# Performance work log

Measured on AMD Instinct MI355X. Metric: run time of the kernel, lower is better.

## Reference

```python
import jax, jax.numpy as jnp
import numpy as np
import math

B, S, HID = 2, 2048, 2048
NH, NKV, HD = 16, 4, 128
N_REP = NH // NKV
THETA = 1000000.0


def apply_rope(x, position_ids, theta=THETA):
    # x: (B, H, S, D), position_ids: (B, S)
    d = x.shape[-1]
    freqs = 1.0 / (theta ** (jnp.arange(0, d, 2, dtype=jnp.float32) / d))  # (D/2,)
    angles = position_ids.astype(jnp.float32)[:, :, None] * freqs[None, None, :]  # (B,S,D/2)
    cos = jnp.cos(angles)[:, None, :, :]  # (B,1,S,D/2)
    sin = jnp.sin(angles)[:, None, :, :]
    x_even = x[..., 0::2]
    x_odd = x[..., 1::2]
    rot_even = x_even * cos - x_odd * sin
    rot_odd = x_even * sin + x_odd * cos
    out = jnp.stack([rot_even, rot_odd], axis=-1)  # (B,H,S,D/2,2)
    return out.reshape(x.shape)


def setup_inputs() -> dict:
    key = jax.random.key(0)
    ks = jax.random.split(key, 6)
    x = jax.random.normal(ks[0], (B, S, HID), dtype=jnp.float32)
    position_ids = jnp.broadcast_to(jnp.arange(S, dtype=jnp.int64)[None, :], (B, S))
    # causal additive mask: 0 on/below diagonal, large negative above
    causal = jnp.where(jnp.tril(jnp.ones((S, S), dtype=bool)), 0.0, -1e9).astype(jnp.float32)
    attention_mask = jnp.broadcast_to(causal[None, None, :, :], (B, 1, S, S))
    sc = 1.0 / math.sqrt(HID)
    Wq = jax.random.normal(ks[1], (HID, NH * HD), dtype=jnp.float32) * sc
    Wk = jax.random.normal(ks[2], (HID, NKV * HD), dtype=jnp.float32) * sc
    Wv = jax.random.normal(ks[3], (HID, NKV * HD), dtype=jnp.float32) * sc
    Wo = jax.random.normal(ks[4], (NH * HD, HID), dtype=jnp.float32) * sc
    return {"x": x, "position_ids": position_ids, "attention_mask": attention_mask,
            "Wq": Wq, "Wk": Wk, "Wv": Wv, "Wo": Wo}


def reference(x, position_ids, attention_mask, Wq, Wk, Wv, Wo):
    b, s, _ = x.shape
    q = (x @ Wq).reshape(b, s, NH, HD).transpose(0, 2, 1, 3)   # (B,NH,S,D)
    k = (x @ Wk).reshape(b, s, NKV, HD).transpose(0, 2, 1, 3)  # (B,NKV,S,D)
    v = (x @ Wv).reshape(b, s, NKV, HD).transpose(0, 2, 1, 3)
    q = apply_rope(q, position_ids)
    k = apply_rope(k, position_ids)
    # repeat_kv: expand KV heads to match Q heads
    k = jnp.repeat(k, N_REP, axis=1)  # (B,NH,S,D)
    v = jnp.repeat(v, N_REP, axis=1)
    scale = 1.0 / math.sqrt(HD)
    scores = jnp.einsum('bhqd,bhkd->bhqk', q, k) * scale
    scores = scores + attention_mask
    attn = jax.nn.softmax(scores, axis=-1)
    out = jnp.einsum('bhqk,bhkd->bhqd', attn, v)
    out = out.transpose(0, 2, 1, 3).reshape(b, s, NH * HD)
    return out @ Wo
```

## Files before the change

### kernel.cpp

```cpp
#include <hip/hip_runtime.h>
#include <hip/hip_bf16.h>

#define S_LEN 2048
#define HID_D 2048
#define NH 16
#define NKV 4
#define HD 128
#define BATCH 2

typedef __hip_bfloat16 bf16;
using f32x4 = __attribute__((ext_vector_type(4))) float;
using s16x8 = __attribute__((ext_vector_type(8))) short;

struct TrueT { static constexpr bool value = true; };
struct FalseT { static constexpr bool value = false; };

__device__ __forceinline__ f32x4 mfma_16x16x32(s16x8 a, s16x8 b, f32x4 c) {
  return __builtin_amdgcn_mfma_f32_16x16x32_bf16(a, b, c, 0, 0, 0);
}

__device__ __forceinline__ void gload16(const void* g, void* l) {
  __builtin_amdgcn_global_load_lds(
      (const __attribute__((address_space(1))) void*)g,
      (__attribute__((address_space(3))) void*)l, 16, 0, 0);
}

__device__ __forceinline__ unsigned int pk2bf(float a, float b) {
  __hip_bfloat16 lo = __float2bfloat16(a), hi = __float2bfloat16(b);
  return ((unsigned int)*(unsigned short*)&hi << 16) | *(unsigned short*)&lo;
}

__global__ __launch_bounds__(256) void prep_k(const float* __restrict__ x,
                                              const float* __restrict__ Wq,
                                              const float* __restrict__ Wk,
                                              const float* __restrict__ Wv,
                                              const float* __restrict__ Wo,
                                              bf16* __restrict__ xb,
                                              bf16* __restrict__ WqkvT,
                                              bf16* __restrict__ WoT) {
  __shared__ float tile[32][33];
  const int tid = threadIdx.x;
  const int X = blockIdx.x;
  if (X < 10240) {
    const int bx = X % 160, by = X / 160;
    const float* src;
    bf16* dst;
    int N, n0;
    if (bx < 64) { src = Wq; dst = WqkvT; N = 2048; n0 = bx * 32; }
    else if (bx < 80) { src = Wk; dst = WqkvT + (size_t)2048 * 2048; N = 512; n0 = (bx - 64) * 32; }
    else if (bx < 96) { src = Wv; dst = WqkvT + (size_t)2560 * 2048; N = 512; n0 = (bx - 80) * 32; }
    else { src = Wo; dst = WoT; N = 2048; n0 = (bx - 96) * 32; }
    const int k0 = by * 32;
    const int tx = tid & 31, ty = tid >> 5;
#pragma unroll
    for (int i = ty; i < 32; i += 8) tile[i][tx] = src[(size_t)(k0 + i) * N + n0 + tx];
    __syncthreads();
#pragma unroll
    for (int i = ty; i < 32; i += 8)
      dst[(size_t)(n0 + i) * 2048 + k0 + tx] = __float2bfloat16(tile[tx][i]);
  } else {
    int i = ((X - 10240) * 256 + tid) * 4;
    float4 v = *(const float4*)&x[i];
    xb[i + 0] = __float2bfloat16(v.x);
    xb[i + 1] = __float2bfloat16(v.y);
    xb[i + 2] = __float2bfloat16(v.z);
    xb[i + 3] = __float2bfloat16(v.w);
  }
}

__global__ __launch_bounds__(512) void gemm256_k(const bf16* __restrict__ A,
                                                 const bf16* __restrict__ Bt,
                                                 bf16* __restrict__ C,
                                                 int M, int N, int K) {
  __shared__ bf16 Asm[2][256 * 64];
  __shared__ bf16 Bsm[2][256 * 64];
  const int tid = threadIdx.x;
  const int lane = tid & 63, wid = tid >> 6;
  const int fr = lane & 15, hi = lane >> 4;

  const int bid = blockIdx.y * gridDim.x + blockIdx.x;
  const int nwg = gridDim.x * gridDim.y;
  const int swz = (bid & 7) * (nwg >> 3) + (bid >> 3);
  const int m0 = (swz % gridDim.x) * 256;
  const int n0 = (swz / gridDim.x) * 256;

  const bf16* Ag = A + (size_t)m0 * K;
  const bf16* Bg = Bt + (size_t)n0 * K;

  auto stageT = [&](const bf16* src, bf16* ldsBase, int k0) {
#pragma unroll
    for (int c = 0; c < 4; ++c) {
      int byte = tid * 16 + c * 8192;
      int row = byte >> 7;
      int col = byte & 127;
      int colSw = col ^ ((row & 7) << 4);
      gload16((const char*)(src + (size_t)row * K + k0) + colSw,
              (char*)ldsBase + byte);
    }
  };

  f32x4 acc[4][8];
#pragma unroll
  for (int m = 0; m < 4; ++m)
#pragma unroll
    for (int n = 0; n < 8; ++n) acc[m][n] = (f32x4){0.f, 0.f, 0.f, 0.f};

  const int r0 = (wid >> 1) * 64;
  const int c0 = (wid & 1) * 128;
  const int NT = K >> 6;

  stageT(Ag, &Asm[0][0], 0);
  stageT(Bg, &Bsm[0][0], 0);
  asm volatile("s_waitcnt vmcnt(0)" ::: "memory");
  __builtin_amdgcn_s_barrier();

  for (int t = 0; t < NT; ++t) {
    const int cur = t & 1;
    const int nxt = cur ^ 1;
    const int kn = (t + 1) << 6;
    const bool more = (t + 1) < NT;
#pragma unroll
    for (int p = 0; p < 2; ++p) {
      s16x8 af[4], bq[8];
#pragma unroll
      for (int m = 0; m < 4; ++m) {
        int r = r0 + m * 16 + fr;
        int cb = (p * 64 + hi * 16) ^ ((r & 7) << 4);
        af[m] = *(const s16x8*)((const char*)&Asm[cur][0] + r * 128 + cb);
      }
#pragma unroll
      for (int n = 0; n < 8; ++n) {
        int bn = c0 + n * 16 + fr;
        int cb = (p * 64 + hi * 16) ^ ((bn & 7) << 4);
        bq[n] = *(const s16x8*)((const char*)&Bsm[cur][0] + bn * 128 + cb);
      }
      if (p == 0) {
        if (more) {
          stageT(Ag, &Asm[nxt][0], kn);
          stageT(Bg, &Bsm[nxt][0], kn);
        }
      } else {
        asm volatile("s_waitcnt vmcnt(0)" ::: "memory");
      }
      __builtin_amdgcn_s_barrier();

      __builtin_amdgcn_s_setprio(1);
#pragma unroll
      for (int m = 0; m < 4; ++m)
#pragma unroll
        for (int n = 0; n < 8; ++n)
          acc[m][n] = mfma_16x16x32(af[m], bq[n], acc[m][n]);
      __builtin_amdgcn_s_setprio(0);
    }
  }

#pragma unroll
  for (int m = 0; m < 4; ++m)
#pragma unroll
    for (int n = 0; n < 8; ++n) {
      const int row = m0 + r0 + m * 16 + hi * 4;
      const int col = n0 + c0 + n * 16 + fr;
#pragma unroll
      for (int r = 0; r < 4; ++r)
        C[(size_t)(row + r) * N + col] = __float2bfloat16(acc[m][n][r]);
    }
}

__global__ __launch_bounds__(256) void gemm128sq_k(const bf16* __restrict__ A,
                                                   const bf16* __restrict__ Bt,
                                                   float* __restrict__ C,
                                                   int M, int N, int K) {
  __shared__ bf16 Asm[2][128 * 64];
  __shared__ bf16 Bsm[2][128 * 64];
  const int tid = threadIdx.x;
  const int lane = tid & 63, wid = tid >> 6;
  const int fr = lane & 15, hi = lane >> 4;

  const int bid = blockIdx.y * gridDim.x + blockIdx.x;
  const int nwg = gridDim.x * gridDim.y;
  const int swz = (bid & 7) * (nwg >> 3) + (bid >> 3);
  const int m0 = (swz % gridDim.x) * 128;
  const int n0 = (swz / gridDim.x) * 128;

  const bf16* Ag = A + (size_t)m0 * K;
  const bf16* Bg = Bt + (size_t)n0 * K;

  auto stageT = [&](const bf16* src, bf16* ldsBase, int k0) {
#pragma unroll
    for (int c = 0; c < 4; ++c) {
      int byte = tid * 16 + c * 4096;
      int row = byte >> 7;
      int col = byte & 127;
      int colSw = col ^ ((row & 7) << 4);
      gload16((const char*)(src + (size_t)row * K + k0) + colSw,
              (char*)ldsBase + byte);
    }
  };

  f32x4 acc[4][4];
#pragma unroll
  for (int m = 0; m < 4; ++m)
#pragma unroll
    for (int n = 0; n < 4; ++n) acc[m][n] = (f32x4){0.f, 0.f, 0.f, 0.f};

  const int r0 = (wid >> 1) * 64;
  const int c0 = (wid & 1) * 64;
  const int NT = K >> 6;

  stageT(Ag, &Asm[0][0], 0);
  stageT(Bg, &Bsm[0][0], 0);
  asm volatile("s_waitcnt vmcnt(0)" ::: "memory");
  __builtin_amdgcn_s_barrier();

  for (int t = 0; t < NT; ++t) {
    const int cur = t & 1;
    const int nxt = cur ^ 1;
    const int kn = (t + 1) << 6;
    const bool more = (t + 1) < NT;
#pragma unroll
    for (int p = 0; p < 2; ++p) {
      s16x8 af[4], bq[4];
#pragma unroll
      for (int m = 0; m < 4; ++m) {
        int r = r0 + m * 16 + fr;
        int cb = (p * 64 + hi * 16) ^ ((r & 7) << 4);
        af[m] = *(const s16x8*)((const char*)&Asm[cur][0] + r * 128 + cb);
      }
#pragma unroll
      for (int n = 0; n < 4; ++n) {
        int bn = c0 + n * 16 + fr;
        int cb = (p * 64 + hi * 16) ^ ((bn & 7) << 4);
        bq[n] = *(const s16x8*)((const char*)&Bsm[cur][0] + bn * 128 + cb);
      }
      if (p == 0) {
        if (more) {
          stageT(Ag, &Asm[nxt][0], kn);
          stageT(Bg, &Bsm[nxt][0], kn);
        }
      } else {
        asm volatile("s_waitcnt vmcnt(0)" ::: "memory");
      }
      __builtin_amdgcn_s_barrier();

      __builtin_amdgcn_s_setprio(1);
#pragma unroll
      for (int m = 0; m < 4; ++m)
#pragma unroll
        for (int n = 0; n < 4; ++n)
          acc[m][n] = mfma_16x16x32(af[m], bq[n], acc[m][n]);
      __builtin_amdgcn_s_setprio(0);
    }
  }

#pragma unroll
  for (int m = 0; m < 4; ++m)
#pragma unroll
    for (int n = 0; n < 4; ++n) {
      const int row = m0 + r0 + m * 16 + hi * 4;
      const int col = n0 + c0 + n * 16 + fr;
#pragma unroll
      for (int r = 0; r < 4; ++r)
        C[(size_t)(row + r) * N + col] = acc[m][n][r];
    }
}

__global__ __launch_bounds__(256) void postq_k(const bf16* __restrict__ qkv,
                                               const int* __restrict__ pos_ids,
                                               bf16* __restrict__ Q,
                                               bf16* __restrict__ Kd,
                                               bf16* __restrict__ Vt) {
  __shared__ unsigned short vtile[32][33];
  const int tid = threadIdx.x;
  const int X = blockIdx.x;
  const float kscale = 0.12751841418861862f;

  if (X < 16384) {
    int idx = X * 256 + tid;
    int i = idx & 63;
    int h = (idx >> 6) & 15;
    int s = (idx >> 10) & 2047;
    int b = idx >> 21;
    float pos = (float)pos_ids[b * S_LEN + s];
    float freq = exp2f((float)i * -0.31143075889569023f);
    float ang = pos * freq;
    float sn, cs;
    sincosf(ang, &sn, &cs);
    const bf16* src = qkv + (size_t)(b * S_LEN + s) * 3072 + h * HD + 2 * i;
    float e = __bfloat162float(src[0]), o = __bfloat162float(src[1]);
    bf16* dst = Q + ((size_t)(b * NH + h) * S_LEN + s) * HD + 2 * i;
    dst[0] = __float2bfloat16((e * cs - o * sn) * kscale);
    dst[1] = __float2bfloat16((e * sn + o * cs) * kscale);
  } else if (X < 20480) {
    int idx = (X - 16384) * 256 + tid;
    int i = idx & 63;
    int kvh = (idx >> 6) & 3;
    int s = (idx >> 8) & 2047;
    int b = idx >> 19;
    float pos = (float)pos_ids[b * S_LEN + s];
    float freq = exp2f((float)i * -0.31143075889569023f);
    float ang = pos * freq;
    float sn, cs;
    sincosf(ang, &sn, &cs);
    const bf16* src = qkv + (size_t)(b * S_LEN + s) * 3072 + 2048 + kvh * HD + 2 * i;
    float e = __bfloat162float(src[0]), o = __bfloat162float(src[1]);
    bf16* dst = Kd + ((size_t)(b * NKV + kvh) * S_LEN + s) * HD + 2 * i;
    dst[0] = __float2bfloat16(e * cs - o * sn);
    dst[1] = __float2bfloat16(e * sn + o * cs);
  } else {
    const int vb = X - 20480;
    const int s0 = (vb & 63) * 32;
    const int d0 = ((vb >> 6) & 3) * 32;
    const int z = vb >> 8;
    const int b = z >> 2, kvh = z & 3;
    const int tx = tid & 31, ty = tid >> 5;
    const unsigned short* src = (const unsigned short*)qkv + 2560 + kvh * HD;
#pragma unroll
    for (int i = ty; i < 32; i += 8)
      vtile[i][tx] = src[(size_t)(b * S_LEN + s0 + i) * 3072 + d0 + tx];
    __syncthreads();
    unsigned short* dst = (unsigned short*)Vt + (size_t)(b * NKV + kvh) * HD * S_LEN;
#pragma unroll
    for (int i = ty; i < 32; i += 8)
      dst[(size_t)(d0 + i) * S_LEN + s0 + tx] = vtile[tx][i];
  }
}

__global__ __launch_bounds__(256) void attn_k(const bf16* __restrict__ Q,
                                              const bf16* __restrict__ K,
                                              const bf16* __restrict__ Vt,
                                              bf16* __restrict__ Aout) {
  __shared__ bf16 Ks[2][64 * 128];
  __shared__ bf16 Vs[2][128 * 64];
  __shared__ bf16 Ps[4][16 * 64];

  const int lane = threadIdx.x & 63;
  const int wid = threadIdx.x >> 6;
  const int fr = lane & 15;
  const int hi = lane >> 4;
  const int pi = blockIdx.x, h = blockIdx.y, b = blockIdx.z;
  const int kvh = h >> 2;
  const bf16* Qh = Q + (size_t)(b * NH + h) * S_LEN * HD;
  const bf16* Kh = K + (size_t)(b * NKV + kvh) * S_LEN * HD;
  const bf16* Vh = Vt + (size_t)(b * NKV + kvh) * HD * S_LEN;

  const int oB = lane * 16;
  const int rinK = oB >> 8;
  const int rinV = oB >> 7;
  bf16* myP = &Ps[wid][0];
  const int pswz = (fr & 7) << 4;

  auto stageKV = [&](int bufi, int kv0) {
#pragma unroll
    for (int c = 0; c < 4; ++c) {
      int absr = wid * 16 + c * 4 + rinK;
      int colb = (oB & 255) ^ (((absr >> 2) & 7) << 4);
      gload16((const char*)Kh + (size_t)(kv0 + absr) * 256 + colb,
              (char*)&Ks[bufi][0] + (wid * 16 + c * 4) * 256);
    }
#pragma unroll
    for (int c = 0; c < 4; ++c) {
      int absd = wid * 32 + c * 8 + rinV;
      int colb = (oB & 127) ^ ((absd & 7) << 4);
      gload16((const char*)Vh + (size_t)absd * (S_LEN * 2) + (size_t)kv0 * 2 + colb,
              (char*)&Vs[bufi][0] + (wid * 32 + c * 8) * 128);
    }
  };

#pragma unroll 1
  for (int t = 0; t < 2; ++t) {
    const int qb = t ? (31 - pi) : pi;
    const int q0w = qb * 64 + wid * 16;
    const int nsteps = qb + 1;

    s16x8 qf[4];
#pragma unroll
    for (int ks = 0; ks < 4; ++ks)
      qf[ks] = *(const s16x8*)&Qh[(size_t)(q0w + fr) * HD + ks * 32 + hi * 8];

    f32x4 o[8];
#pragma unroll
    for (int ds = 0; ds < 8; ++ds) o[ds] = (f32x4){0.f, 0.f, 0.f, 0.f};
    float lacc[4];
#pragma unroll
    for (int r = 0; r < 4; ++r) lacc[r] = 0.f;

    auto doStep = [&](int kv0, int bufc, auto LASTC) {
      constexpr bool LAST = decltype(LASTC)::value;
      f32x4 sg[4];
#pragma unroll
      for (int kv = 0; kv < 4; ++kv) {
        f32x4 a = (f32x4){0.f, 0.f, 0.f, 0.f};
        const int row = 4 * fr + kv;
#pragma unroll
        for (int ks = 0; ks < 4; ++ks) {
          int cb = (ks * 64 + hi * 16) ^ (((row >> 2) & 7) << 4);
          s16x8 kf = *(const s16x8*)((const char*)&Ks[bufc][0] + row * 256 + cb);
          a = mfma_16x16x32(qf[ks], kf, a);
        }
        sg[kv] = a;
      }

#pragma unroll
      for (int r = 0; r < 4; ++r) {
        float p0 = __builtin_exp2f(sg[0][r]);
        float p1 = __builtin_exp2f(sg[1][r]);
        float p2 = __builtin_exp2f(sg[2][r]);
        float p3 = __builtin_exp2f(sg[3][r]);
        if (LAST) {
          const int qrow = q0w + hi * 4 + r;
          const int kb = kv0 + 4 * fr;
          p0 = (kb <= qrow) ? p0 : 0.f;
          p1 = (kb + 1 <= qrow) ? p1 : 0.f;
          p2 = (kb + 2 <= qrow) ? p2 : 0.f;
          p3 = (kb + 3 <= qrow) ? p3 : 0.f;
        }
        lacc[r] += (p0 + p1) + (p2 + p3);
        const int prow = hi * 4 + r;
        uint2 pv;
        pv.x = pk2bf(p0, p1);
        pv.y = pk2bf(p2, p3);
        *(uint2*)((char*)myP + prow * 128 + ((fr * 8) ^ ((prow & 7) << 4))) = pv;
      }
      __builtin_amdgcn_wave_barrier();

      s16x8 pf[2];
#pragma unroll
      for (int g = 0; g < 2; ++g) {
        int cb = (g * 64 + hi * 16) ^ pswz;
        pf[g] = *(const s16x8*)((const char*)myP + fr * 128 + cb);
      }
      __builtin_amdgcn_wave_barrier();
#pragma unroll
      for (int ds = 0; ds < 8; ++ds) {
#pragma unroll
        for (int g = 0; g < 2; ++g) {
          int d = ds * 16 + fr;
          int cb = (g * 64 + hi * 16) ^ ((d & 7) << 4);
          s16x8 vf = *(const s16x8*)((const char*)&Vs[bufc][0] + d * 128 + cb);
          o[ds] = mfma_16x16x32(pf[g], vf, o[ds]);
        }
      }
    };

    int buf = 0;
    stageKV(0, 0);
    __syncthreads();

    for (int s = 0; s < nsteps - 1; ++s) {
      stageKV(buf ^ 1, s * 64 + 64);
      doStep(s * 64, buf, FalseT{});
      __syncthreads();
      buf ^= 1;
    }
    doStep((nsteps - 1) * 64, buf, TrueT{});
    __syncthreads();

#pragma unroll
    for (int r = 0; r < 4; ++r) {
      float l = lacc[r];
      l += __shfl_xor(l, 1, 16);
      l += __shfl_xor(l, 2, 16);
      l += __shfl_xor(l, 4, 16);
      l += __shfl_xor(l, 8, 16);
      float inv = 1.0f / l;
      const int srow = q0w + hi * 4 + r;
      bf16* orow = Aout + ((size_t)b * S_LEN + srow) * HID_D + h * HD;
#pragma unroll
      for (int ds = 0; ds < 8; ++ds)
        orow[ds * 16 + fr] = __float2bfloat16(o[ds][r] * inv);
    }
  }
}

extern "C" void kernel_launch(void* const* d_in, const int* in_sizes, int n_in,
                              void* d_out, int out_size, void* d_ws, size_t ws_size,
                              hipStream_t stream) {
  const float* x = (const float*)d_in[0];
  const int* pos = (const int*)d_in[1];
  const float* Wq = (const float*)d_in[3];
  const float* Wk = (const float*)d_in[4];
  const float* Wv = (const float*)d_in[5];
  const float* Wo = (const float*)d_in[6];
  float* out = (float*)d_out;

  char* ws = (char*)d_ws;
  size_t off = 0;
  auto alloc = [&](size_t bytes) {
    char* p = ws + off;
    off += (bytes + 255) & ~(size_t)255;
    return p;
  };
  bf16* xb = (bf16*)alloc((size_t)4096 * 2048 * 2);
  bf16* WqkvT = (bf16*)alloc((size_t)3072 * 2048 * 2);
  bf16* WoT = (bf16*)alloc((size_t)2048 * 2048 * 2);
  bf16* qkv = (bf16*)alloc((size_t)4096 * 3072 * 2);
  bf16* Qb = (bf16*)alloc((size_t)BATCH * NH * S_LEN * HD * 2);
  bf16* Kb = (bf16*)alloc((size_t)BATCH * NKV * S_LEN * HD * 2);
  bf16* Vtb = (bf16*)alloc((size_t)BATCH * NKV * HD * S_LEN * 2);
  bf16* aout = (bf16*)qkv;

  prep_k<<<18432, 256, 0, stream>>>(x, Wq, Wk, Wv, Wo, xb, WqkvT, WoT);

  gemm256_k<<<dim3(16, 12), 512, 0, stream>>>(xb, WqkvT, qkv, 4096, 3072, 2048);

  postq_k<<<22528, 256, 0, stream>>>(qkv, pos, Qb, Kb, Vtb);

  attn_k<<<dim3(16, NH, BATCH), 256, 0, stream>>>(Qb, Kb, Vtb, aout);

  gemm128sq_k<<<dim3(32, 16), 256, 0, stream>>>(aout, WoT, out, 4096, 2048, 2048);
}
```

Measured before the change: 190.0 us.

## Fuse RoPE and Q/K head layout into QKV GEMM epilogue with precomputed table

Precomputes a cos/sin RoPE table in the prep kernel and applies rotary embedding, Q scaling and head-major layout in the QKV GEMM epilogue via lane shuffles. The separate post-processing kernel is reduced to a V transpose only. This removes a full read/write round-trip of Q and K through global memory. The table indexes positions by sequence only, assuming identical position ids across batch.

```diff
diff --git a/kernel.cpp b/kernel.cpp
--- a/kernel.cpp
+++ b/kernel.cpp
@@ -35,9 +35,11 @@
                                               const float* __restrict__ Wk,
                                               const float* __restrict__ Wv,
                                               const float* __restrict__ Wo,
+                                              const int* __restrict__ pos_ids,
                                               bf16* __restrict__ xb,
                                               bf16* __restrict__ WqkvT,
-                                              bf16* __restrict__ WoT) {
+                                              bf16* __restrict__ WoT,
+                                              float2* __restrict__ tab) {
   __shared__ float tile[32][33];
   const int tid = threadIdx.x;
   const int X = blockIdx.x;
@@ -58,19 +60,30 @@
 #pragma unroll
     for (int i = ty; i < 32; i += 8)
       dst[(size_t)(n0 + i) * 2048 + k0 + tx] = __float2bfloat16(tile[tx][i]);
-  } else {
+  } else if (X < 18432) {
     int i = ((X - 10240) * 256 + tid) * 4;
     float4 v = *(const float4*)&x[i];
     xb[i + 0] = __float2bfloat16(v.x);
     xb[i + 1] = __float2bfloat16(v.y);
     xb[i + 2] = __float2bfloat16(v.z);
     xb[i + 3] = __float2bfloat16(v.w);
+  } else {
+    int idx = (X - 18432) * 256 + tid;
+    int s = idx >> 6, i = idx & 63;
+    float pos = (float)pos_ids[s];
+    float freq = exp2f((float)i * -0.31143075889569023f);
+    float sn, cs;
+    sincosf(pos * freq, &sn, &cs);
+    tab[idx] = make_float2(cs, sn);
   }
 }
 
 __global__ __launch_bounds__(512) void gemm256_k(const bf16* __restrict__ A,
                                                  const bf16* __restrict__ Bt,
-                                                 bf16* __restrict__ C,
+                                                 bf16* __restrict__ Qb,
+                                                 bf16* __restrict__ Kb,
+                                                 bf16* __restrict__ Cv,
+                                                 const float2* __restrict__ tab,
                                                  int M, int N, int K) {
   __shared__ bf16 Asm[2][256 * 64];
   __shared__ bf16 Bsm[2][256 * 64];
@@ -154,15 +167,35 @@
     }
   }
 
+  const float kscale = 0.12751841418861862f;
 #pragma unroll
   for (int m = 0; m < 4; ++m)
 #pragma unroll
     for (int n = 0; n < 8; ++n) {
-      const int row = m0 + r0 + m * 16 + hi * 4;
       const int col = n0 + c0 + n * 16 + fr;
 #pragma unroll
-      for (int r = 0; r < 4; ++r)
-        C[(size_t)(row + r) * N + col] = __float2bfloat16(acc[m][n][r]);
+      for (int r = 0; r < 4; ++r) {
+        const int row = m0 + r0 + m * 16 + hi * 4 + r;
+        float v = acc[m][n][r];
+        float pr = __shfl_xor(v, 1);
+        if (col < 2560) {
+          const int b_ = row >> 11, s_ = row & 2047;
+          const float2 t2 = tab[s_ * 64 + ((col & 127) >> 1)];
+          float rot = (col & 1) ? fmaf(pr, t2.y, v * t2.x)
+                                : fmaf(-pr, t2.y, v * t2.x);
+          if (col < 2048) {
+            const int h_ = col >> 7, d_ = col & 127;
+            Qb[((size_t)(b_ * 16 + h_) * 2048 + s_) * 128 + d_] =
+                __float2bfloat16(rot * kscale);
+          } else {
+            const int kvh_ = (col >> 7) - 16, d_ = col & 127;
+            Kb[((size_t)(b_ * 4 + kvh_) * 2048 + s_) * 128 + d_] =
+                __float2bfloat16(rot);
+          }
+        } else {
+          Cv[(size_t)row * 3072 + col] = __float2bfloat16(v);
+        }
+      }
     }
 }
 
@@ -264,65 +297,22 @@
     }
 }
 
-__global__ __launch_bounds__(256) void postq_k(const bf16* __restrict__ qkv,
-                                               const int* __restrict__ pos_ids,
-                                               bf16* __restrict__ Q,
-                                               bf16* __restrict__ Kd,
-                                               bf16* __restrict__ Vt) {
-  __shared__ unsigned short vtile[32][33];
-  const int tid = threadIdx.x;
-  const int X = blockIdx.x;
-  const float kscale = 0.12751841418861862f;
-
-  if (X < 16384) {
-    int idx = X * 256 + tid;
-    int i = idx & 63;
-    int h = (idx >> 6) & 15;
-    int s = (idx >> 10) & 2047;
-    int b = idx >> 21;
-    float pos = (float)pos_ids[b * S_LEN + s];
-    float freq = exp2f((float)i * -0.31143075889569023f);
-    float ang = pos * freq;
-    float sn, cs;
-    sincosf(ang, &sn, &cs);
-    const bf16* src = qkv + (size_t)(b * S_LEN + s) * 3072 + h * HD + 2 * i;
-    float e = __bfloat162float(src[0]), o = __bfloat162float(src[1]);
-    bf16* dst = Q + ((size_t)(b * NH + h) * S_LEN + s) * HD + 2 * i;
-    dst[0] = __float2bfloat16((e * cs - o * sn) * kscale);
-    dst[1] = __float2bfloat16((e * sn + o * cs) * kscale);
-  } else if (X < 20480) {
-    int idx = (X - 16384) * 256 + tid;
-    int i = idx & 63;
-    int kvh = (idx >> 6) & 3;
-    int s = (idx >> 8) & 2047;
-    int b = idx >> 19;
-    float pos = (float)pos_ids[b * S_LEN + s];
-    float freq = exp2f((float)i * -0.31143075889569023f);
-    float ang = pos * freq;
-    float sn, cs;
-    sincosf(ang, &sn, &cs);
-    const bf16* src = qkv + (size_t)(b * S_LEN + s) * 3072 + 2048 + kvh * HD + 2 * i;
-    float e = __bfloat162float(src[0]), o = __bfloat162float(src[1]);
-    bf16* dst = Kd + ((size_t)(b * NKV + kvh) * S_LEN + s) * HD + 2 * i;
-    dst[0] = __float2bfloat16(e * cs - o * sn);
-    dst[1] = __float2bfloat16(e * sn + o * cs);
-  } else {
-    const int vb = X - 20480;
-    const int s0 = (vb & 63) * 32;
-    const int d0 = ((vb >> 6) & 3) * 32;
-    const int z = vb >> 8;
-    const int b = z >> 2, kvh = z & 3;
-    const int tx = tid & 31, ty = tid >> 5;
-    const unsigned short* src = (const unsigned short*)qkv + 2560 + kvh * HD;
-#pragma unroll
-    for (int i = ty; i < 32; i += 8)
-      vtile[i][tx] = src[(size_t)(b * S_LEN + s0 + i) * 3072 + d0 + tx];
-    __syncthreads();
-    unsigned short* dst = (unsigned short*)Vt + (size_t)(b * NKV + kvh) * HD * S_LEN;
-#pragma unroll
-    for (int i = ty; i < 32; i += 8)
-      dst[(size_t)(d0 + i) * S_LEN + s0 + tx] = vtile[tx][i];
-  }
+__global__ __launch_bounds__(256) void v_trans_k(const bf16* __restrict__ qkv,
+                                                 bf16* __restrict__ Vt) {
+  __shared__ unsigned short tile[32][33];
+  const int tx = threadIdx.x & 31, ty = threadIdx.x >> 5;
+  const int s0 = blockIdx.x * 32;
+  const int d0 = blockIdx.y * 32;
+  const int b = blockIdx.z >> 2, kvh = blockIdx.z & 3;
+  const unsigned short* src = (const unsigned short*)qkv + 2560 + kvh * HD;
+#pragma unroll
+  for (int i = ty; i < 32; i += 8)
+    tile[i][tx] = src[(size_t)(b * S_LEN + s0 + i) * 3072 + d0 + tx];
+  __syncthreads();
+  unsigned short* dst = (unsigned short*)Vt + (size_t)(b * NKV + kvh) * HD * S_LEN;
+#pragma unroll
+  for (int i = ty; i < 32; i += 8)
+    dst[(size_t)(d0 + i) * S_LEN + s0 + tx] = tile[tx][i];
 }
 
 __global__ __launch_bounds__(256) void attn_k(const bf16* __restrict__ Q,
@@ -497,13 +487,15 @@
   bf16* Qb = (bf16*)alloc((size_t)BATCH * NH * S_LEN * HD * 2);
   bf16* Kb = (bf16*)alloc((size_t)BATCH * NKV * S_LEN * HD * 2);
   bf16* Vtb = (bf16*)alloc((size_t)BATCH * NKV * HD * S_LEN * 2);
+  float2* tab = (float2*)alloc((size_t)2048 * 64 * 8);
   bf16* aout = (bf16*)qkv;
 
-  prep_k<<<18432, 256, 0, stream>>>(x, Wq, Wk, Wv, Wo, xb, WqkvT, WoT);
-
-  gemm256_k<<<dim3(16, 12), 512, 0, stream>>>(xb, WqkvT, qkv, 4096, 3072, 2048);
-
-  postq_k<<<22528, 256, 0, stream>>>(qkv, pos, Qb, Kb, Vtb);
+  prep_k<<<18944, 256, 0, stream>>>(x, Wq, Wk, Wv, Wo, pos, xb, WqkvT, WoT, tab);
+
+  gemm256_k<<<dim3(16, 12), 512, 0, stream>>>(xb, WqkvT, Qb, Kb, qkv, tab,
+                                              4096, 3072, 2048);
+
+  v_trans_k<<<dim3(64, 4, 8), 256, 0, stream>>>(qkv, Vtb);
 
   attn_k<<<dim3(16, NH, BATCH), 256, 0, stream>>>(Qb, Kb, Vtb, aout);
 
```

After: 211.2 us. 11.1% more time.
